# Optimization experiments

Measured on AMD Instinct MI355X. Metric: run time of the kernel, lower is better.

## Reference

```python
import jax, jax.numpy as jnp
import numpy as np
from jax import lax

B, T, L = 16, 256, 1024       # batch, seq_length, input_size
NF = 32                        # num_filters
KS = [3, 5, 7]                 # kernel_sizes
H = 1024                       # feature_size
GRU_IN = NF * len(KS)          # 96


def setup_inputs() -> dict:
    key = jax.random.key(0)
    ks = jax.random.split(key, 20)
    def rn(k, shape, scale):
        return (jax.random.normal(k, shape, dtype=jnp.float32) * scale)
    inp = {
        "x": jax.random.normal(ks[0], (B, T, L), dtype=jnp.float32),
        "conv_w3": rn(ks[1], (NF, 1, 3), (2.0 / 3) ** 0.5),
        "conv_b3": jnp.zeros((NF,), jnp.float32),
        "conv_w5": rn(ks[2], (NF, 1, 5), (2.0 / 5) ** 0.5),
        "conv_b5": jnp.zeros((NF,), jnp.float32),
        "conv_w7": rn(ks[3], (NF, 1, 7), (2.0 / 7) ** 0.5),
        "conv_b7": jnp.zeros((NF,), jnp.float32),
        "gru_w_ih": rn(ks[4], (3 * H, GRU_IN), GRU_IN ** -0.5),
        "gru_w_hh": rn(ks[5], (3 * H, H), H ** -0.5),
        "gru_b_ih": jnp.zeros((3 * H,), jnp.float32),
        "gru_b_hh": jnp.zeros((3 * H,), jnp.float32),
        "attn_w1": rn(ks[6], (H, H), H ** -0.5),
        "attn_b1": jnp.zeros((H,), jnp.float32),
        "attn_w2": rn(ks[7], (1, H), H ** -0.5),
        "attn_b2": jnp.zeros((1,), jnp.float32),
        "fi_w1": rn(ks[8], (H, H), H ** -0.5),
        "fi_b1": jnp.zeros((H,), jnp.float32),
        "fi_w2": rn(ks[9], (H, H), H ** -0.5),
        "fi_b2": jnp.zeros((H,), jnp.float32),
        "lateral": jnp.full((H, H), 0.1, jnp.float32),
    }
    return inp


def _forward(x, conv_w3, conv_b3, conv_w5, conv_b5, conv_w7, conv_b7,
             gru_w_ih, gru_w_hh, gru_b_ih, gru_b_hh,
             attn_w1, attn_b1, attn_w2, attn_b2,
             fi_w1, fi_b1, fi_w2, fi_b2, lateral):
    b, t, l = x.shape
    # --- per-timestep conv branches (no cross-time dependence -> vectorize over B*T) ---
    xt = x.reshape(b * t, 1, l)  # (BT, C=1, L)
    pooled = []
    for w, bias in ((conv_w3, conv_b3), (conv_w5, conv_b5), (conv_w7, conv_b7)):
        y = lax.conv_general_dilated(xt, w, (1,), "SAME",
                                     dimension_numbers=("NCH", "OIH", "NCH"))
        y = jax.nn.relu(y + bias[None, :, None])
        pooled.append(jnp.max(y, axis=-1))  # adaptive_max_pool1d -> (BT, NF)
    feat = jnp.concatenate(pooled, axis=1).reshape(b, t, -1)  # (B, T, 3*NF)

    # --- GRU over time (sequential carry) ---
    gates_x = jnp.einsum("bti,gi->btg", feat, gru_w_ih) + gru_b_ih  # (B,T,3H)

    def step(h, gx):
        gh = h @ gru_w_hh.T + gru_b_hh
        xr, xz, xn = jnp.split(gx, 3, axis=-1)
        hr, hz, hn = jnp.split(gh, 3, axis=-1)
        r = jax.nn.sigmoid(xr + hr)
        z = jax.nn.sigmoid(xz + hz)
        n = jnp.tanh(xn + r * hn)
        h_new = (1.0 - z) * n + z * h
        return h_new, h_new

    h0 = jnp.zeros((b, gru_w_hh.shape[1]), x.dtype)
    _, hs = lax.scan(step, h0, jnp.swapaxes(gates_x, 0, 1))  # (T,B,H)
    hs = jnp.swapaxes(hs, 0, 1)  # (B,T,H)

    # --- attention: per-step softmax over a length-1 axis -> weights are all 1 ---
    scores = jnp.tanh(hs @ attn_w1.T + attn_b1) @ attn_w2.T + attn_b2  # (B,T,1)
    attn = jax.nn.softmax(scores, axis=-1)  # softmax over singleton seq dim -> ones
    attended = hs * attn  # (B,T,H)

    # --- lateral inhibition + feature integration MLP ---
    inhib = attended - jax.nn.relu(jnp.einsum("bth,hf->btf", attended, lateral))
    features = jax.nn.relu(inhib @ fi_w1.T + fi_b1) @ fi_w2.T + fi_b2  # (B,T,H)
    return features, attn[..., 0]  # attention_weights (B,T)


def reference(x, conv_w3, conv_b3, conv_w5, conv_b5, conv_w7, conv_b7,
              gru_w_ih, gru_w_hh, gru_b_ih, gru_b_hh,
              attn_w1, attn_b1, attn_w2, attn_b2,
              fi_w1, fi_b1, fi_w2, fi_b2, lateral):
    return _forward(x, conv_w3, conv_b3, conv_w5, conv_b5, conv_w7, conv_b7,
                    gru_w_ih, gru_w_hh, gru_b_ih, gru_b_hh,
                    attn_w1, attn_b1, attn_w2, attn_b2,
                    fi_w1, fi_b1, fi_w2, fi_b2, lateral)
```

## Files before the change

### kernel.cpp

```cpp
#include <hip/hip_runtime.h>
#include <stdint.h>
#include <stddef.h>

#define B_   16
#define T_   256
#define L_   1024
#define H_   1024
#define G3_  3072
#define KIN_ 96

#define SENT_     0x7FC1
#define SENT_X2_  0x7FC17FC1u

typedef __attribute__((ext_vector_type(8))) __bf16 bf16x8;
typedef __attribute__((ext_vector_type(4))) float  f32x4;
typedef __attribute__((ext_vector_type(4))) int    i32x4;

static __device__ __forceinline__ unsigned short f2bf(float x) {
  unsigned int u = __builtin_bit_cast(unsigned int, x);
  u += 0x7FFFu + ((u >> 16) & 1u);
  return (unsigned short)(u >> 16);
}
static __device__ __forceinline__ float bf2f(unsigned short s) {
  unsigned int u = ((unsigned int)s) << 16;
  return __builtin_bit_cast(float, u);
}

__global__ void cvt4_kernel(const float* __restrict__ s0, unsigned short* __restrict__ d0,
                            const float* __restrict__ s1, unsigned short* __restrict__ d1,
                            const float* __restrict__ s2, unsigned short* __restrict__ d2,
                            const float* __restrict__ s3, unsigned short* __restrict__ d3) {
  const int n0 = G3_ * H_;
  const int n1 = n0 + G3_ * KIN_;
  const int n2 = n1 + H_ * H_;
  const int n3 = n2 + H_ * H_;
  int i = blockIdx.x * 256 + threadIdx.x;
  const int stride = gridDim.x * 256;
  for (; i < n3; i += stride) {
    if (i < n0)      d0[i]      = f2bf(s0[i]);
    else if (i < n1) d1[i - n0] = f2bf(s1[i - n0]);
    else if (i < n2) d2[i - n1] = f2bf(s2[i - n1]);
    else             d3[i - n2] = f2bf(s3[i - n2]);
  }
}

__global__ void transpose_bf16_kernel(const float* __restrict__ in,
                                      unsigned short* __restrict__ out,
                                      int R, int C) {
  int i = blockIdx.x * 256 + threadIdx.x;
  int n = R * C, stride = gridDim.x * 256;
  for (; i < n; i += stride) {
    int r = i / C, c = i % C;
    out[(size_t)c * R + r] = f2bf(in[i]);
  }
}

__global__ void ones_kernel(float* __restrict__ p, int n) {
  int i = blockIdx.x * 256 + threadIdx.x;
  if (i < n) p[i] = 1.0f;
}

__global__ void fill_sent_kernel(unsigned int* __restrict__ p, int n) {
  int i = blockIdx.x * 256 + threadIdx.x;
  const int stride = gridDim.x * 256;
  const unsigned int v = SENT_X2_;
  for (; i < n; i += stride) {
    unsigned int* q = p + i;
    asm volatile("global_store_dword %0, %1, off sc0 sc1" :: "v"(q), "v"(v) : "memory");
  }
}

__global__ __launch_bounds__(256) void conv_kernel(
    const float* __restrict__ x,
    const float* __restrict__ w3, const float* __restrict__ b3,
    const float* __restrict__ w5, const float* __restrict__ b5,
    const float* __restrict__ w7, const float* __restrict__ b7,
    unsigned short* __restrict__ feat) {
  __shared__ float xpad[L_ + 8];
  __shared__ float wlds[96][8];
  __shared__ float blds[96];
  __shared__ float wmax[4][96];
  const int tid = threadIdx.x;
  const int rid = blockIdx.x;
  const int b = rid >> 8;
  const int t = rid & 255;
  const float* xr = x + (size_t)rid * L_;
  for (int off = tid; off < L_; off += 256) xpad[off + 3] = xr[off];
  if (tid < 3) xpad[tid] = 0.f;
  if (tid >= 3 && tid < 8) xpad[L_ + tid] = 0.f;
  if (tid < 96) {
    const int f = tid;
    float wv[8];
#pragma unroll
    for (int k = 0; k < 8; ++k) wv[k] = 0.f;
    float bv;
    if (f < 32)      { for (int k = 0; k < 3; ++k) wv[k + 2] = w3[f * 3 + k]; bv = b3[f]; }
    else if (f < 64) { int ff = f - 32; for (int k = 0; k < 5; ++k) wv[k + 1] = w5[ff * 5 + k]; bv = b5[ff]; }
    else             { int ff = f - 64; for (int k = 0; k < 7; ++k) wv[k] = w7[ff * 7 + k]; bv = b7[ff]; }
#pragma unroll
    for (int k = 0; k < 8; ++k) wlds[f][k] = wv[k];
    blds[f] = bv;
  }
  __syncthreads();
  const int w = tid >> 6, lane = tid & 63;
  const int p0 = w * 256 + lane * 4;
  float xv[10];
#pragma unroll
  for (int i = 0; i < 10; ++i) xv[i] = xpad[p0 + i];
  for (int f = 0; f < 96; ++f) {
    float a0 = 0.f, a1 = 0.f, a2 = 0.f, a3 = 0.f;
#pragma unroll
    for (int k = 0; k < 7; ++k) {
      const float wk = wlds[f][k];
      a0 = fmaf(wk, xv[k],     a0);
      a1 = fmaf(wk, xv[k + 1], a1);
      a2 = fmaf(wk, xv[k + 2], a2);
      a3 = fmaf(wk, xv[k + 3], a3);
    }
    float m = fmaxf(fmaxf(a0, a1), fmaxf(a2, a3));
#pragma unroll
    for (int d = 1; d < 64; d <<= 1) m = fmaxf(m, __shfl_xor(m, d, 64));
    if (lane == 0) wmax[w][f] = m;
  }
  __syncthreads();
  if (tid < 96) {
    float m = fmaxf(fmaxf(wmax[0][tid], wmax[1][tid]),
                    fmaxf(wmax[2][tid], wmax[3][tid]));
    m += blds[tid];
    m = m > 0.f ? m : 0.f;
    feat[(size_t)(t * B_ + b) * KIN_ + tid] = f2bf(m);
  }
}

template <int EP>
__global__ __launch_bounds__(256) void gemm_kernel(
    const unsigned short* __restrict__ A,
    const unsigned short* __restrict__ Bm,
    int M, int N, int K, int lda, int ldb,
    const float* __restrict__ bias,
    float* __restrict__ outF,
    unsigned short* __restrict__ outB) {
  __shared__ __align__(16) unsigned short As[2][128 * 40];
  __shared__ __align__(16) unsigned short Bs[2][128 * 40];
  const int tid = threadIdx.x;
  const int n0 = blockIdx.x * 128;
  const int m0 = blockIdx.y * 128;
  const int w = tid >> 6;
  const int l = tid & 63;
  const int lr = l & 15;
  const int lk = (l >> 4) * 8;
  const int srow = tid >> 2;
  const int skc = (tid & 3) * 8;

  f32x4 acc[2][8];
#pragma unroll
  for (int i = 0; i < 2; ++i)
#pragma unroll
    for (int j = 0; j < 8; ++j) acc[i][j] = (f32x4){0.f, 0.f, 0.f, 0.f};

  const int NK = K >> 5;
  const unsigned short* Aptr  = A  + (size_t)(m0 + srow)      * lda + skc;
  const unsigned short* Aptr2 = A  + (size_t)(m0 + 64 + srow) * lda + skc;
  const unsigned short* Bptr  = Bm + (size_t)(n0 + srow)      * ldb + skc;
  const unsigned short* Bptr2 = Bm + (size_t)(n0 + 64 + srow) * ldb + skc;

  i32x4 ar0 = *(const i32x4*)(Aptr);
  i32x4 ar1 = *(const i32x4*)(Aptr2);
  i32x4 br0 = *(const i32x4*)(Bptr);
  i32x4 br1 = *(const i32x4*)(Bptr2);
  *(i32x4*)&As[0][srow * 40 + skc]        = ar0;
  *(i32x4*)&As[0][(64 + srow) * 40 + skc] = ar1;
  *(i32x4*)&Bs[0][srow * 40 + skc]        = br0;
  *(i32x4*)&Bs[0][(64 + srow) * 40 + skc] = br1;
  __syncthreads();

  for (int kk = 0; kk < NK; ++kk) {
    const int cur = kk & 1;
    if (kk + 1 < NK) {
      const int ko = (kk + 1) << 5;
      ar0 = *(const i32x4*)(Aptr  + ko);
      ar1 = *(const i32x4*)(Aptr2 + ko);
      br0 = *(const i32x4*)(Bptr  + ko);
      br1 = *(const i32x4*)(Bptr2 + ko);
    }
    const bf16x8 a0 = *(const bf16x8*)&As[cur][(w * 32 + lr) * 40 + lk];
    const bf16x8 a1 = *(const bf16x8*)&As[cur][(w * 32 + 16 + lr) * 40 + lk];
#pragma unroll
    for (int nt = 0; nt < 8; ++nt) {
      const bf16x8 bb = *(const bf16x8*)&Bs[cur][(nt * 16 + lr) * 40 + lk];
      acc[0][nt] = __builtin_amdgcn_mfma_f32_16x16x32_bf16(a0, bb, acc[0][nt], 0, 0, 0);
      acc[1][nt] = __builtin_amdgcn_mfma_f32_16x16x32_bf16(a1, bb, acc[1][nt], 0, 0, 0);
    }
    __syncthreads();
    if (kk + 1 < NK) {
      const int nxt = cur ^ 1;
      *(i32x4*)&As[nxt][srow * 40 + skc]        = ar0;
      *(i32x4*)&As[nxt][(64 + srow) * 40 + skc] = ar1;
      *(i32x4*)&Bs[nxt][srow * 40 + skc]        = br0;
      *(i32x4*)&Bs[nxt][(64 + srow) * 40 + skc] = br1;
    }
    __syncthreads();
  }

#pragma unroll
  for (int mt = 0; mt < 2; ++mt) {
#pragma unroll
    for (int nt = 0; nt < 8; ++nt) {
      const f32x4 v = acc[mt][nt];
      const int gcol = n0 + nt * 16 + lr;
#pragma unroll
      for (int e = 0; e < 4; ++e) {
        const int grow = m0 + w * 32 + mt * 16 + (l >> 4) * 4 + e;
        const float val = v[e];
        if (EP == 0) {
          outF[(size_t)grow * N + gcol] = val + bias[gcol];
        } else if (EP == 1) {
          const float hsv = bf2f(A[(size_t)grow * lda + gcol]);
          outB[(size_t)grow * N + gcol] = f2bf(hsv - fmaxf(val, 0.f));
        } else if (EP == 2) {
          outB[(size_t)grow * N + gcol] = f2bf(fmaxf(val + bias[gcol], 0.f));
        } else {
          const int tt = grow >> 4;
          const int bb2 = grow & 15;
          outF[((size_t)bb2 * T_ + tt) * H_ + gcol] = val + bias[gcol];
        }
      }
    }
  }
}

__global__ __launch_bounds__(256, 1) void gru_scan_kernel(
    const unsigned short* __restrict__ Whh,
    const float* __restrict__ gates,
    const float* __restrict__ bhh,
    unsigned short* __restrict__ hs) {
  __shared__ __align__(16) float ghp[4][3][16][16];
  __shared__ __align__(16) unsigned short hlds[16][16];
  const int tid = threadIdx.x;
  const int g = blockIdx.x;
  const int w = tid >> 6;
  const int l = tid & 63;
  const int lr = l & 15;
  const int lk8 = (l >> 4) * 8;
  const int j0 = g * 16;

  bf16x8 af[3][8];
#pragma unroll
  for (int m = 0; m < 3; ++m) {
    const size_t row = (size_t)(m * H_ + j0 + lr);
#pragma unroll
    for (int kk = 0; kk < 8; ++kk) {
      const int k = w * 256 + kk * 32 + lk8;
      af[m][kk] = *(const bf16x8*)(Whh + row * H_ + k);
    }
  }
  const int jb = tid & 15;
  const int bb = tid >> 4;
  const float bhr = bhh[j0 + jb];
  const float bhz = bhh[H_ + j0 + jb];
  const float bhn = bhh[2 * H_ + j0 + jb];
  float hprev = 0.f;

  for (int t = 0; t < T_; ++t) {
    const size_t grow = ((size_t)t * B_ + bb) * G3_;
    const float gxr = gates[grow + j0 + jb];
    const float gxz = gates[grow + H_ + j0 + jb];
    const float gxn = gates[grow + 2 * H_ + j0 + jb];

    const unsigned short* hp = hs + (size_t)t * (B_ * H_) +
                               (size_t)lr * H_ + w * 256 + lk8;
    i32x4 u0, u1, u2, u3, u4, u5, u6, u7;
    while (true) {
      asm volatile(
          "global_load_dwordx4 %0, %8, off sc0 sc1\n\t"
          "global_load_dwordx4 %1, %8, off offset:64 sc0 sc1\n\t"
          "global_load_dwordx4 %2, %8, off offset:128 sc0 sc1\n\t"
          "global_load_dwordx4 %3, %8, off offset:192 sc0 sc1\n\t"
          "global_load_dwordx4 %4, %8, off offset:256 sc0 sc1\n\t"
          "global_load_dwordx4 %5, %8, off offset:320 sc0 sc1\n\t"
          "global_load_dwordx4 %6, %8, off offset:384 sc0 sc1\n\t"
          "global_load_dwordx4 %7, %8, off offset:448 sc0 sc1\n\t"
          "s_waitcnt vmcnt(0)"
          : "=&v"(u0), "=&v"(u1), "=&v"(u2), "=&v"(u3),
            "=&v"(u4), "=&v"(u5), "=&v"(u6), "=&v"(u7)
          : "v"(hp)
          : "memory");
      const int ok = ((u0[0] & 0xFFFF) != SENT_) & ((u1[0] & 0xFFFF) != SENT_) &
                     ((u2[0] & 0xFFFF) != SENT_) & ((u3[0] & 0xFFFF) != SENT_) &
                     ((u4[0] & 0xFFFF) != SENT_) & ((u5[0] & 0xFFFF) != SENT_) &
                     ((u6[0] & 0xFFFF) != SENT_) & ((u7[0] & 0xFFFF) != SENT_);
      if (__ballot(ok) == ~0ull) break;
    }
    bf16x8 hf[8];
    hf[0] = __builtin_bit_cast(bf16x8, u0);
    hf[1] = __builtin_bit_cast(bf16x8, u1);
    hf[2] = __builtin_bit_cast(bf16x8, u2);
    hf[3] = __builtin_bit_cast(bf16x8, u3);
    hf[4] = __builtin_bit_cast(bf16x8, u4);
    hf[5] = __builtin_bit_cast(bf16x8, u5);
    hf[6] = __builtin_bit_cast(bf16x8, u6);
    hf[7] = __builtin_bit_cast(bf16x8, u7);

    f32x4 C0 = (f32x4){0.f, 0.f, 0.f, 0.f}, C1 = C0, C2 = C0;
#pragma unroll
    for (int kk = 0; kk < 8; ++kk) {
      C0 = __builtin_amdgcn_mfma_f32_16x16x32_bf16(af[0][kk], hf[kk], C0, 0, 0, 0);
      C1 = __builtin_amdgcn_mfma_f32_16x16x32_bf16(af[1][kk], hf[kk], C1, 0, 0, 0);
      C2 = __builtin_amdgcn_mfma_f32_16x16x32_bf16(af[2][kk], hf[kk], C2, 0, 0, 0);
    }
    const int rbase = (l >> 4) * 4;
    *(f32x4*)&ghp[w][0][lr][rbase] = C0;
    *(f32x4*)&ghp[w][1][lr][rbase] = C1;
    *(f32x4*)&ghp[w][2][lr][rbase] = C2;
    __syncthreads();

    const float ghr = ghp[0][0][bb][jb] + ghp[1][0][bb][jb] +
                      ghp[2][0][bb][jb] + ghp[3][0][bb][jb] + bhr;
    const float ghz = ghp[0][1][bb][jb] + ghp[1][1][bb][jb] +
                      ghp[2][1][bb][jb] + ghp[3][1][bb][jb] + bhz;
    const float ghn = ghp[0][2][bb][jb] + ghp[1][2][bb][jb] +
                      ghp[2][2][bb][jb] + ghp[3][2][bb][jb] + bhn;
    const float r = 1.f / (1.f + __expf(-(gxr + ghr)));
    const float z = 1.f / (1.f + __expf(-(gxz + ghz)));
    const float xn = gxn + r * ghn;
    const float n = 2.f / (1.f + __expf(-2.f * xn)) - 1.f;
    const float hnew = (1.f - z) * n + z * hprev;
    hprev = hnew;
    hlds[bb][jb] = f2bf(hnew);
    __syncthreads();

    if (tid < 32) {
      const int bb2 = tid >> 1, half = tid & 1;
      unsigned short* sp = hs + ((size_t)(t + 1) * B_ + bb2) * H_ + j0 + half * 8;
      const i32x4 v = *(const i32x4*)&hlds[bb2][half * 8];
      asm volatile("global_store_dwordx4 %0, %1, off sc0 sc1"
                   :: "v"(sp), "v"(v) : "memory");
    }
  }
}

extern "C" void kernel_launch(void* const* d_in, const int* in_sizes, int n_in,
                              void* d_out, int out_size, void* d_ws, size_t ws_size,
                              hipStream_t stream) {
  (void)in_sizes; (void)n_in; (void)out_size; (void)ws_size;
  const float* x    = (const float*)d_in[0];
  const float* w3   = (const float*)d_in[1];
  const float* b3   = (const float*)d_in[2];
  const float* w5   = (const float*)d_in[3];
  const float* b5   = (const float*)d_in[4];
  const float* w7   = (const float*)d_in[5];
  const float* b7   = (const float*)d_in[6];
  const float* wih  = (const float*)d_in[7];
  const float* whh  = (const float*)d_in[8];
  const float* bih  = (const float*)d_in[9];
  const float* bhh  = (const float*)d_in[10];
  const float* fiw1 = (const float*)d_in[15];
  const float* fib1 = (const float*)d_in[16];
  const float* fiw2 = (const float*)d_in[17];
  const float* fib2 = (const float*)d_in[18];
  const float* lat  = (const float*)d_in[19];

  char* ws = (char*)d_ws;
  size_t off = 0;
  auto alloc = [&](size_t bytes) -> void* {
    void* p = ws + off;
    off += (bytes + 255) & ~(size_t)255;
    return p;
  };
  unsigned short* whh_bf  = (unsigned short*)alloc((size_t)G3_ * H_ * 2);
  unsigned short* wih_bf  = (unsigned short*)alloc((size_t)G3_ * KIN_ * 2);
  unsigned short* latT_bf = (unsigned short*)alloc((size_t)H_ * H_ * 2);
  unsigned short* fiw1_bf = (unsigned short*)alloc((size_t)H_ * H_ * 2);
  unsigned short* fiw2_bf = (unsigned short*)alloc((size_t)H_ * H_ * 2);
  unsigned short* feat_bf = (unsigned short*)alloc((size_t)B_ * T_ * KIN_ * 2);
  float*          gates   = (float*)alloc((size_t)B_ * T_ * G3_ * 4);
  unsigned short* hsbuf   = (unsigned short*)alloc((size_t)(T_ + 1) * B_ * H_ * 2);
  unsigned short* inhib   = (unsigned short*)alloc((size_t)B_ * T_ * H_ * 2);
  unsigned short* y1      = (unsigned short*)alloc((size_t)B_ * T_ * H_ * 2);

  hipMemsetAsync(hsbuf, 0, (size_t)B_ * H_ * 2, stream);
  fill_sent_kernel<<<1024, 256, 0, stream>>>(
      (unsigned int*)(hsbuf + (size_t)B_ * H_), T_ * B_ * H_ / 2);

  cvt4_kernel<<<2048, 256, 0, stream>>>(whh, whh_bf, wih, wih_bf,
                                        fiw1, fiw1_bf, fiw2, fiw2_bf);
  transpose_bf16_kernel<<<1024, 256, 0, stream>>>(lat, latT_bf, H_, H_);

  conv_kernel<<<B_ * T_, 256, 0, stream>>>(x, w3, b3, w5, b5, w7, b7, feat_bf);

  {
    dim3 grid(G3_ / 128, (B_ * T_) / 128);
    gemm_kernel<0><<<grid, 256, 0, stream>>>(feat_bf, wih_bf, B_ * T_, G3_, KIN_,
                                             KIN_, KIN_, bih, gates, nullptr);
  }

  gru_scan_kernel<<<64, 256, 0, stream>>>(whh_bf, gates, bhh, hsbuf);

  const unsigned short* hs1 = hsbuf + (size_t)B_ * H_;
  {
    dim3 grid(H_ / 128, (B_ * T_) / 128);
    gemm_kernel<1><<<grid, 256, 0, stream>>>(hs1, latT_bf, B_ * T_, H_, H_,
                                             H_, H_, nullptr, nullptr, inhib);
    gemm_kernel<2><<<grid, 256, 0, stream>>>(inhib, fiw1_bf, B_ * T_, H_, H_,
                                             H_, H_, fib1, nullptr, y1);
    gemm_kernel<3><<<grid, 256, 0, stream>>>(y1, fiw2_bf, B_ * T_, H_, H_,
                                             H_, H_, fib2, (float*)d_out, nullptr);
  }

  ones_kernel<<<16, 256, 0, stream>>>((float*)d_out + (size_t)B_ * T_ * H_, B_ * T_);
}
```

Before: 1.081 ms.

## Split GRU scan K-reduction across 8 waves and drop second barrier per step

The persistent GRU scan kernel now uses 512 threads (8 waves), each handling a 128-wide K slice, so each wave holds fewer Whh fragments and polls a shorter h slice. The partial-sum LDS buffer is double-buffered and padded, which removes the second __syncthreads per timestep. Each thread now stores its own bf16 h element directly to global memory instead of staging it through LDS. The sentinel check now tests every 16-bit element with a bit trick rather than only the first. In exchange there are more partial sums to reduce, and there are now scalar global stores, which risks partial-visibility handling that the full-element sentinel check is meant to cover.

```diff
diff --git a/kernel.cpp b/kernel.cpp
--- a/kernel.cpp
+++ b/kernel.cpp
@@ -24,6 +24,10 @@
 static __device__ __forceinline__ float bf2f(unsigned short s) {
   unsigned int u = ((unsigned int)s) << 16;
   return __builtin_bit_cast(float, u);
+}
+static __device__ __forceinline__ unsigned sentmask(unsigned d) {
+  const unsigned x = d ^ SENT_X2_;
+  return (x - 0x00010001u) & ~x & 0x80008000u;
 }
 
 __global__ void cvt4_kernel(const float* __restrict__ s0, unsigned short* __restrict__ d0,
@@ -229,13 +233,12 @@
   }
 }
 
-__global__ __launch_bounds__(256, 1) void gru_scan_kernel(
+__global__ __launch_bounds__(512, 2) void gru_scan_kernel(
     const unsigned short* __restrict__ Whh,
     const float* __restrict__ gates,
     const float* __restrict__ bhh,
     unsigned short* __restrict__ hs) {
-  __shared__ __align__(16) float ghp[4][3][16][16];
-  __shared__ __align__(16) unsigned short hlds[16][16];
+  __shared__ float ghp[2][8][3][16][17];
   const int tid = threadIdx.x;
   const int g = blockIdx.x;
   const int w = tid >> 6;
@@ -244,16 +247,41 @@
   const int lk8 = (l >> 4) * 8;
   const int j0 = g * 16;
 
-  bf16x8 af[3][8];
-#pragma unroll
-  for (int m = 0; m < 3; ++m) {
-    const size_t row = (size_t)(m * H_ + j0 + lr);
-#pragma unroll
-    for (int kk = 0; kk < 8; ++kk) {
-      const int k = w * 256 + kk * 32 + lk8;
-      af[m][kk] = *(const bf16x8*)(Whh + row * H_ + k);
-    }
-  }
+  const unsigned short* ap0 = Whh + (size_t)(j0 + lr) * H_ + w * 128 + lk8;
+  const unsigned short* ap1 = ap0 + (size_t)H_ * H_;
+  const unsigned short* ap2 = ap1 + (size_t)H_ * H_;
+  i32x4 w00, w01, w02, w03, w10, w11, w12, w13, w20, w21, w22, w23;
+  asm volatile(
+      "global_load_dwordx4 %0,  %12, off\n\t"
+      "global_load_dwordx4 %1,  %12, off offset:64\n\t"
+      "global_load_dwordx4 %2,  %12, off offset:128\n\t"
+      "global_load_dwordx4 %3,  %12, off offset:192\n\t"
+      "global_load_dwordx4 %4,  %13, off\n\t"
+      "global_load_dwordx4 %5,  %13, off offset:64\n\t"
+      "global_load_dwordx4 %6,  %13, off offset:128\n\t"
+      "global_load_dwordx4 %7,  %13, off offset:192\n\t"
+      "global_load_dwordx4 %8,  %14, off\n\t"
+      "global_load_dwordx4 %9,  %14, off offset:64\n\t"
+      "global_load_dwordx4 %10, %14, off offset:128\n\t"
+      "global_load_dwordx4 %11, %14, off offset:192\n\t"
+      "s_waitcnt vmcnt(0)"
+      : "=&v"(w00), "=&v"(w01), "=&v"(w02), "=&v"(w03),
+        "=&v"(w10), "=&v"(w11), "=&v"(w12), "=&v"(w13),
+        "=&v"(w20), "=&v"(w21), "=&v"(w22), "=&v"(w23)
+      : "v"(ap0), "v"(ap1), "v"(ap2));
+  const bf16x8 af00 = __builtin_bit_cast(bf16x8, w00);
+  const bf16x8 af01 = __builtin_bit_cast(bf16x8, w01);
+  const bf16x8 af02 = __builtin_bit_cast(bf16x8, w02);
+  const bf16x8 af03 = __builtin_bit_cast(bf16x8, w03);
+  const bf16x8 af10 = __builtin_bit_cast(bf16x8, w10);
+  const bf16x8 af11 = __builtin_bit_cast(bf16x8, w11);
+  const bf16x8 af12 = __builtin_bit_cast(bf16x8, w12);
+  const bf16x8 af13 = __builtin_bit_cast(bf16x8, w13);
+  const bf16x8 af20 = __builtin_bit_cast(bf16x8, w20);
+  const bf16x8 af21 = __builtin_bit_cast(bf16x8, w21);
+  const bf16x8 af22 = __builtin_bit_cast(bf16x8, w22);
+  const bf16x8 af23 = __builtin_bit_cast(bf16x8, w23);
+
   const int jb = tid & 15;
   const int bb = tid >> 4;
   const float bhr = bhh[j0 + jb];
@@ -262,79 +290,81 @@
   float hprev = 0.f;
 
   for (int t = 0; t < T_; ++t) {
-    const size_t grow = ((size_t)t * B_ + bb) * G3_;
-    const float gxr = gates[grow + j0 + jb];
-    const float gxz = gates[grow + H_ + j0 + jb];
-    const float gxn = gates[grow + 2 * H_ + j0 + jb];
+    const int buf = t & 1;
+    float gxr = 0.f, gxz = 0.f, gxn = 0.f;
+    if (tid < 256) {
+      const size_t grow = ((size_t)t * B_ + bb) * G3_;
+      gxr = gates[grow + j0 + jb];
+      gxz = gates[grow + H_ + j0 + jb];
+      gxn = gates[grow + 2 * H_ + j0 + jb];
+    }
 
     const unsigned short* hp = hs + (size_t)t * (B_ * H_) +
-                               (size_t)lr * H_ + w * 256 + lk8;
-    i32x4 u0, u1, u2, u3, u4, u5, u6, u7;
+                               (size_t)lr * H_ + w * 128 + lk8;
+    i32x4 u0, u1, u2, u3;
     while (true) {
       asm volatile(
-          "global_load_dwordx4 %0, %8, off sc0 sc1\n\t"
-          "global_load_dwordx4 %1, %8, off offset:64 sc0 sc1\n\t"
-          "global_load_dwordx4 %2, %8, off offset:128 sc0 sc1\n\t"
-          "global_load_dwordx4 %3, %8, off offset:192 sc0 sc1\n\t"
-          "global_load_dwordx4 %4, %8, off offset:256 sc0 sc1\n\t"
-          "global_load_dwordx4 %5, %8, off offset:320 sc0 sc1\n\t"
-          "global_load_dwordx4 %6, %8, off offset:384 sc0 sc1\n\t"
-          "global_load_dwordx4 %7, %8, off offset:448 sc0 sc1\n\t"
+          "global_load_dwordx4 %0, %4, off sc0 sc1\n\t"
+          "global_load_dwordx4 %1, %4, off offset:64 sc0 sc1\n\t"
+          "global_load_dwordx4 %2, %4, off offset:128 sc0 sc1\n\t"
+          "global_load_dwordx4 %3, %4, off offset:192 sc0 sc1\n\t"
           "s_waitcnt vmcnt(0)"
-          : "=&v"(u0), "=&v"(u1), "=&v"(u2), "=&v"(u3),
-            "=&v"(u4), "=&v"(u5), "=&v"(u6), "=&v"(u7)
+          : "=&v"(u0), "=&v"(u1), "=&v"(u2), "=&v"(u3)
           : "v"(hp)
           : "memory");
-      const int ok = ((u0[0] & 0xFFFF) != SENT_) & ((u1[0] & 0xFFFF) != SENT_) &
-                     ((u2[0] & 0xFFFF) != SENT_) & ((u3[0] & 0xFFFF) != SENT_) &
-                     ((u4[0] & 0xFFFF) != SENT_) & ((u5[0] & 0xFFFF) != SENT_) &
-                     ((u6[0] & 0xFFFF) != SENT_) & ((u7[0] & 0xFFFF) != SENT_);
-      if (__ballot(ok) == ~0ull) break;
-    }
-    bf16x8 hf[8];
-    hf[0] = __builtin_bit_cast(bf16x8, u0);
-    hf[1] = __builtin_bit_cast(bf16x8, u1);
-    hf[2] = __builtin_bit_cast(bf16x8, u2);
-    hf[3] = __builtin_bit_cast(bf16x8, u3);
-    hf[4] = __builtin_bit_cast(bf16x8, u4);
-    hf[5] = __builtin_bit_cast(bf16x8, u5);
-    hf[6] = __builtin_bit_cast(bf16x8, u6);
-    hf[7] = __builtin_bit_cast(bf16x8, u7);
+      const unsigned bad =
+          sentmask(u0[0]) | sentmask(u0[1]) | sentmask(u0[2]) | sentmask(u0[3]) |
+          sentmask(u1[0]) | sentmask(u1[1]) | sentmask(u1[2]) | sentmask(u1[3]) |
+          sentmask(u2[0]) | sentmask(u2[1]) | sentmask(u2[2]) | sentmask(u2[3]) |
+          sentmask(u3[0]) | sentmask(u3[1]) | sentmask(u3[2]) | sentmask(u3[3]);
+      if (__ballot(bad == 0) == ~0ull) break;
+    }
+    const bf16x8 hf0 = __builtin_bit_cast(bf16x8, u0);
+    const bf16x8 hf1 = __builtin_bit_cast(bf16x8, u1);
+    const bf16x8 hf2 = __builtin_bit_cast(bf16x8, u2);
+    const bf16x8 hf3 = __builtin_bit_cast(bf16x8, u3);
 
     f32x4 C0 = (f32x4){0.f, 0.f, 0.f, 0.f}, C1 = C0, C2 = C0;
-#pragma unroll
-    for (int kk = 0; kk < 8; ++kk) {
-      C0 = __builtin_amdgcn_mfma_f32_16x16x32_bf16(af[0][kk], hf[kk], C0, 0, 0, 0);
-      C1 = __builtin_amdgcn_mfma_f32_16x16x32_bf16(af[1][kk], hf[kk], C1, 0, 0, 0);
-      C2 = __builtin_amdgcn_mfma_f32_16x16x32_bf16(af[2][kk], hf[kk], C2, 0, 0, 0);
-    }
-    const int rbase = (l >> 4) * 4;
-    *(f32x4*)&ghp[w][0][lr][rbase] = C0;
-    *(f32x4*)&ghp[w][1][lr][rbase] = C1;
-    *(f32x4*)&ghp[w][2][lr][rbase] = C2;
+    C0 = __builtin_amdgcn_mfma_f32_16x16x32_bf16(af00, hf0, C0, 0, 0, 0);
+    C1 = __builtin_amdgcn_mfma_f32_16x16x32_bf16(af10, hf0, C1, 0, 0, 0);
+    C2 = __builtin_amdgcn_mfma_f32_16x16x32_bf16(af20, hf0, C2, 0, 0, 0);
+    C0 = __builtin_amdgcn_mfma_f32_16x16x32_bf16(af01, hf1, C0, 0, 0, 0);
+    C1 = __builtin_amdgcn_mfma_f32_16x16x32_bf16(af11, hf1, C1, 0, 0, 0);
+    C2 = __builtin_amdgcn_mfma_f32_16x16x32_bf16(af21, hf1, C2, 0, 0, 0);
+    C0 = __builtin_amdgcn_mfma_f32_16x16x32_bf16(af02, hf2, C0, 0, 0, 0);
+    C1 = __builtin_amdgcn_mfma_f32_16x16x32_bf16(af12, hf2, C1, 0, 0, 0);
+    C2 = __builtin_amdgcn_mfma_f32_16x16x32_bf16(af22, hf2, C2, 0, 0, 0);
+    C0 = __builtin_amdgcn_mfma_f32_16x16x32_bf16(af03, hf3, C0, 0, 0, 0);
+    C1 = __builtin_amdgcn_mfma_f32_16x16x32_bf16(af13, hf3, C1, 0, 0, 0);
+    C2 = __builtin_amdgcn_mfma_f32_16x16x32_bf16(af23, hf3, C2, 0, 0, 0);
+
+    const int rb = (l >> 4) * 4;
+#pragma unroll
+    for (int e = 0; e < 4; ++e) {
+      ghp[buf][w][0][lr][rb + e] = C0[e];
+      ghp[buf][w][1][lr][rb + e] = C1[e];
+      ghp[buf][w][2][lr][rb + e] = C2[e];
+    }
     __syncthreads();
 
-    const float ghr = ghp[0][0][bb][jb] + ghp[1][0][bb][jb] +
-                      ghp[2][0][bb][jb] + ghp[3][0][bb][jb] + bhr;
-    const float ghz = ghp[0][1][bb][jb] + ghp[1][1][bb][jb] +
-                      ghp[2][1][bb][jb] + ghp[3][1][bb][jb] + bhz;
-    const float ghn = ghp[0][2][bb][jb] + ghp[1][2][bb][jb] +
-                      ghp[2][2][bb][jb] + ghp[3][2][bb][jb] + bhn;
-    const float r = 1.f / (1.f + __expf(-(gxr + ghr)));
-    const float z = 1.f / (1.f + __expf(-(gxz + ghz)));
-    const float xn = gxn + r * ghn;
-    const float n = 2.f / (1.f + __expf(-2.f * xn)) - 1.f;
-    const float hnew = (1.f - z) * n + z * hprev;
-    hprev = hnew;
-    hlds[bb][jb] = f2bf(hnew);
-    __syncthreads();
-
-    if (tid < 32) {
-      const int bb2 = tid >> 1, half = tid & 1;
-      unsigned short* sp = hs + ((size_t)(t + 1) * B_ + bb2) * H_ + j0 + half * 8;
-      const i32x4 v = *(const i32x4*)&hlds[bb2][half * 8];
-      asm volatile("global_store_dwordx4 %0, %1, off sc0 sc1"
-                   :: "v"(sp), "v"(v) : "memory");
+    if (tid < 256) {
+      float sr = bhr, sz = bhz, sn = bhn;
+#pragma unroll
+      for (int w2 = 0; w2 < 8; ++w2) {
+        sr += ghp[buf][w2][0][bb][jb];
+        sz += ghp[buf][w2][1][bb][jb];
+        sn += ghp[buf][w2][2][bb][jb];
+      }
+      const float r = 1.f / (1.f + __expf(-(gxr + sr)));
+      const float z = 1.f / (1.f + __expf(-(gxz + sz)));
+      const float xn = gxn + r * sn;
+      const float n = 2.f / (1.f + __expf(-2.f * xn)) - 1.f;
+      const float hnew = (1.f - z) * n + z * hprev;
+      hprev = hnew;
+      unsigned short* sp = hs + ((size_t)(t + 1) * B_ + bb) * H_ + j0 + jb;
+      const unsigned hv = (unsigned)f2bf(hnew);
+      asm volatile("global_store_short %0, %1, off sc0 sc1"
+                   :: "v"(sp), "v"(hv) : "memory");
     }
   }
 }
@@ -394,7 +424,7 @@
                                              KIN_, KIN_, bih, gates, nullptr);
   }
 
-  gru_scan_kernel<<<64, 256, 0, stream>>>(whh_bf, gates, bhh, hsbuf);
+  gru_scan_kernel<<<64, 512, 0, stream>>>(whh_bf, gates, bhh, hsbuf);
 
   const unsigned short* hs1 = hsbuf + (size_t)B_ * H_;
   {
```

Result: faster. 1.031 ms (-4.6%).
